# Kernel tuning notes

Hardware: AMD Instinct MI355X
Metric: run time of the kernel (lower is better)

## Reference

```python
import jax, jax.numpy as jnp
import numpy as np

N = 50000
E = 200000
DIMS = [3, 64, 64, 64, 128, 1024, 512, 256, 2]  # hard-coded layer widths from __init__


def setup_inputs() -> dict:
    key = jax.random.key(0)
    ks = jax.random.split(key, 2 + 2 * 8)
    inp = {}
    inp["x"] = jax.random.normal(ks[0], (N, DIMS[0]), dtype=jnp.float32)
    inp["edge_index"] = jax.random.randint(ks[1], (2, E), 0, N, dtype=jnp.int32)
    for i in range(8):
        w = jax.random.normal(ks[2 + 2 * i], (DIMS[i], DIMS[i + 1]), dtype=jnp.float32) / np.sqrt(DIMS[i]).astype(np.float32)
        b = jax.random.normal(ks[3 + 2 * i], (DIMS[i + 1],), dtype=jnp.float32) * 0.01
        inp[f"W{i}"] = w
        inp[f"b{i}"] = b
    return inp


def _gcn_layer(x, row, col, norm, W, b, n):
    # PyG GCNConv: h = x @ W; out_i = sum_{j->i} norm_ij * h_j; out += b
    h = x @ W                          # [N, F_out]
    msg = h[row] * norm[:, None]       # [E+N, F_out] gather + scale
    out = jax.ops.segment_sum(msg, col, num_segments=n)  # scatter-add
    return out + b


def reference(x, edge_index, W0, b0, W1, b1, W2, b2, W3, b3, W4, b4, W5, b5, W6, b6, W7, b7):
    n = x.shape[0]
    # add self-loops (GCNConv default add_self_loops=True)
    loops = jnp.arange(n, dtype=edge_index.dtype)
    row = jnp.concatenate([edge_index[0], loops])  # source nodes
    col = jnp.concatenate([edge_index[1], loops])  # target nodes
    # symmetric degree normalization: deg counts incoming edges at col
    deg = jax.ops.segment_sum(jnp.ones_like(col, dtype=x.dtype), col, num_segments=n)
    dis = jnp.where(deg > 0, jax.lax.rsqrt(jnp.maximum(deg, 1e-12)), 0.0)
    norm = dis[row] * dis[col]  # [E+N]

    Ws = [W0, W1, W2, W3, W4, W5, W6, W7]
    bs = [b0, b1, b2, b3, b4, b5, b6, b7]
    # dropout is identity in eval mode (training=False)
    for i in range(7):
        x = jax.nn.relu(_gcn_layer(x, row, col, norm, Ws[i], bs[i], n))
    x = _gcn_layer(x, row, col, norm, Ws[7], bs[7], n)
    return x
```

## Files before the change

kernel.cpp:

```cpp
#include <hip/hip_runtime.h>
#include <hip/hip_bf16.h>

typedef __hip_bfloat16 bf16;
typedef __attribute__((ext_vector_type(8))) short short8;
typedef __attribute__((ext_vector_type(4))) float floatx4;

__device__ inline float ldf(const float* p, size_t i) { return p[i]; }
__device__ inline float ldf(const bf16* p, size_t i) { return (float)p[i]; }
__device__ inline void stf(float* p, size_t i, float v) { p[i] = v; }
__device__ inline void stf(bf16* p, size_t i, float v) { p[i] = (bf16)v; }

__device__ inline void async16(const bf16* g, bf16* l) {
    __builtin_amdgcn_global_load_lds(
        (const __attribute__((address_space(1))) void*)g,
        (__attribute__((address_space(3))) void*)l, 16, 0, 0);
}

__device__ inline void loadvec(const float* __restrict__ p, float* d) {
    float4 v = *(const float4*)p;
    d[0] = v.x; d[1] = v.y; d[2] = v.z; d[3] = v.w;
}
__device__ inline void loadvec(const bf16* __restrict__ p, float* d) {
    uint4 u = *(const uint4*)p;
    const unsigned* w = (const unsigned*)&u;
    #pragma unroll
    for (int j = 0; j < 4; ++j) {
        d[2 * j]     = __uint_as_float(w[j] << 16);
        d[2 * j + 1] = __uint_as_float(w[j] & 0xffff0000u);
    }
}
template <int VEC, typename TOut>
__device__ inline void storevec(TOut* __restrict__ p, const float* d) {
    if constexpr (sizeof(TOut) == 4) {
        #pragma unroll
        for (int j = 0; j < VEC; j += 4) {
            float4 v = {d[j], d[j + 1], d[j + 2], d[j + 3]};
            *(float4*)(p + j) = v;
        }
    } else {
        unsigned w[VEC / 2];
        #pragma unroll
        for (int j = 0; j < VEC / 2; ++j) {
            bf16 lo = (bf16)d[2 * j], hi = (bf16)d[2 * j + 1];
            w[j] = ((unsigned)*(unsigned short*)&hi << 16) | (unsigned)*(unsigned short*)&lo;
        }
        if constexpr (VEC == 8) *(uint4*)p = *(uint4*)&w[0];
        else                    *(uint2*)p = *(uint2*)&w[0];
    }
}

__global__ void detect_dtype_kernel(const unsigned short* __restrict__ x, int* __restrict__ flag) {
    __shared__ float s[256];
    float m = 0.0f;
    for (int i = threadIdx.x; i < 512; i += 256) {
        unsigned int u = ((unsigned int)x[i]) << 16;
        float v = __uint_as_float(u);
        if (!isnan(v)) m = fmaxf(m, fabsf(v));
    }
    s[threadIdx.x] = m;
    __syncthreads();
    for (int o = 128; o > 0; o >>= 1) {
        if (threadIdx.x < (unsigned)o) s[threadIdx.x] = fmaxf(s[threadIdx.x], s[threadIdx.x + o]);
        __syncthreads();
    }
    if (threadIdx.x == 0) flag[0] = (s[0] > 1e3f) ? 0 : 1;
}

struct CvtJobs {
    const void* src[14];
    float* dst[14];
    int off[15];
    int cnt;
};
__global__ void cvt_fused_kernel(CvtJobs j, const int* __restrict__ flag) {
    int t = blockIdx.x * 256 + threadIdx.x;
    if (t >= j.off[j.cnt]) return;
    int k = 0;
    while (t >= j.off[k + 1]) ++k;
    int e = t - j.off[k];
    float v = *flag ? (float)((const bf16*)j.src[k])[e] : ((const float*)j.src[k])[e];
    j.dst[k][e] = v;
}

struct WtJobs {
    const void* src[3];
    bf16* dst[3];
    int K[3], N[3];
    int off[4];
};
__global__ void wt_fused_kernel(WtJobs j, const int* __restrict__ flag) {
    int t = blockIdx.x * 256 + threadIdx.x;
    if (t >= j.off[3]) return;
    int k_ = 0;
    while (t >= j.off[k_ + 1]) ++k_;
    int e = t - j.off[k_];
    int K = j.K[k_], Nn = j.N[k_];
    int n = e / K, kk = e % K;
    size_t si = (size_t)kk * Nn + n;
    float v = *flag ? (float)((const bf16*)j.src[k_])[si] : ((const float*)j.src[k_])[si];
    j.dst[k_][e] = (bf16)v;
}

__global__ void zero_int_kernel(int* a, int n) {
    int i = blockIdx.x * blockDim.x + threadIdx.x;
    if (i < n) a[i] = 0;
}

__global__ void hist_kernel(const int* __restrict__ col, int* __restrict__ counts, int E) {
    int e = blockIdx.x * blockDim.x + threadIdx.x;
    if (e < E) atomicAdd(&counts[col[e]], 1);
}

__global__ void scan_reduce_kernel(const int* __restrict__ counts, int* __restrict__ bs, int n) {
    __shared__ int s[1024];
    int i = blockIdx.x * 1024 + threadIdx.x;
    s[threadIdx.x] = (i < n) ? counts[i] : 0;
    __syncthreads();
    for (int o = 512; o > 0; o >>= 1) {
        if (threadIdx.x < (unsigned)o) s[threadIdx.x] += s[threadIdx.x + o];
        __syncthreads();
    }
    if (threadIdx.x == 0) bs[blockIdx.x] = s[0];
}

__global__ void scan_blocksums_kernel(int* __restrict__ bs, int nb) {
    __shared__ int s[1024];
    int v = (threadIdx.x < (unsigned)nb) ? bs[threadIdx.x] : 0;
    s[threadIdx.x] = v;
    __syncthreads();
    for (int off = 1; off < 1024; off <<= 1) {
        int t = (threadIdx.x >= (unsigned)off) ? s[threadIdx.x - off] : 0;
        __syncthreads();
        s[threadIdx.x] += t;
        __syncthreads();
    }
    if (threadIdx.x < (unsigned)nb) bs[threadIdx.x] = s[threadIdx.x] - v;
}

__global__ void scan_final_kernel(int* __restrict__ counts, const int* __restrict__ bs,
                                  int* __restrict__ offsets, float* __restrict__ dis, int n) {
    __shared__ int s[1024];
    int i = blockIdx.x * 1024 + threadIdx.x;
    int v = (i < n) ? counts[i] : 0;
    if (i < n) { dis[i] = rsqrtf((float)(v + 1)); counts[i] = 0; }
    s[threadIdx.x] = v;
    __syncthreads();
    for (int off = 1; off < 1024; off <<= 1) {
        int t = (threadIdx.x >= (unsigned)off) ? s[threadIdx.x - off] : 0;
        __syncthreads();
        s[threadIdx.x] += t;
        __syncthreads();
    }
    if (i < n) offsets[i + 1] = s[threadIdx.x] + bs[blockIdx.x];
    if (i == 0) offsets[0] = 0;
}

__global__ void fill_kernel(const int* __restrict__ row, const int* __restrict__ col,
                            const int* __restrict__ offsets, int* __restrict__ cursor,
                            int2* __restrict__ csr_sw, const float* __restrict__ dis, int E) {
    int e = blockIdx.x * blockDim.x + threadIdx.x;
    if (e < E) {
        int d = col[e];
        int s = row[e];
        int pos = offsets[d] + atomicAdd(&cursor[d], 1);
        csr_sw[pos] = make_int2(s, __float_as_int(dis[s]));
    }
}

template <typename TIn, typename TOut>
__global__ void agg_kernel(const TIn* __restrict__ h, const int* __restrict__ offsets,
                           const int2* __restrict__ csr_sw, const float* __restrict__ dis,
                           const float* __restrict__ bias, TOut* __restrict__ out,
                           int n, int F, int add_bias, int relu) {
    long long idx = (long long)blockIdx.x * blockDim.x + threadIdx.x;
    long long total = (long long)n * F;
    if (idx >= total) return;
    int i = (int)(idx / F);
    int f = (int)(idx % F);
    float di = dis[i];
    float acc = di * ldf(h, (size_t)i * F + f);
    float acc2 = 0.0f;
    int e0 = offsets[i], e1 = offsets[i + 1];
    int e = e0;
    for (; e + 1 < e1; e += 2) {
        int2 sw0 = csr_sw[e];
        int2 sw1 = csr_sw[e + 1];
        float v0 = ldf(h, (size_t)sw0.x * F + f);
        float v1 = ldf(h, (size_t)sw1.x * F + f);
        acc  += __int_as_float(sw0.y) * v0;
        acc2 += __int_as_float(sw1.y) * v1;
    }
    if (e < e1) {
        int2 sw = csr_sw[e];
        acc += __int_as_float(sw.y) * ldf(h, (size_t)sw.x * F + f);
    }
    acc = (acc + acc2) * di;
    if (add_bias) acc += bias[f];
    if (relu) acc = fmaxf(acc, 0.0f);
    stf(out, (size_t)idx, acc);
}

__global__ void agg2_out_kernel(const float* __restrict__ in, const int* __restrict__ offsets,
                                const int2* __restrict__ csr_sw, const float* __restrict__ dis,
                                const float* __restrict__ bias, void* __restrict__ out,
                                int n, const int* __restrict__ flag) {
    int idx = blockIdx.x * 256 + threadIdx.x;
    if (idx >= n * 2) return;
    int i = idx >> 1;
    int f = idx & 1;
    float di = dis[i];
    float acc = di * in[idx];
    float acc2 = 0.0f;
    int e0 = offsets[i], e1 = offsets[i + 1];
    int e = e0;
    for (; e + 1 < e1; e += 2) {
        int2 sw0 = csr_sw[e];
        int2 sw1 = csr_sw[e + 1];
        float v0 = in[(size_t)sw0.x * 2 + f];
        float v1 = in[(size_t)sw1.x * 2 + f];
        acc  += __int_as_float(sw0.y) * v0;
        acc2 += __int_as_float(sw1.y) * v1;
    }
    if (e < e1) {
        int2 sw = csr_sw[e];
        acc += __int_as_float(sw.y) * in[(size_t)sw.x * 2 + f];
    }
    acc = (acc + acc2) * di + bias[f];
    if (*flag) ((bf16*)out)[idx] = (bf16)acc;
    else       ((float*)out)[idx] = acc;
}

template <int F, int DO_BIAS, int DO_RELU, typename TIn, typename TOut>
__global__ __launch_bounds__(256) void agg_vec_kernel(
        const TIn* __restrict__ h, const int* __restrict__ offsets,
        const int2* __restrict__ csr_sw, const float* __restrict__ dis,
        const float* __restrict__ bias, TOut* __restrict__ out, int n) {
    constexpr int VEC = 16 / sizeof(TIn);
    constexpr int CPL = F / VEC;
    int t = blockIdx.x * 256 + threadIdx.x;
    if (t >= n * CPL) return;
    int i = t / CPL;
    int c = t % CPL;
    int fbase = c * VEC;
    float di = dis[i];
    float acc[VEC], acc2[VEC];
    loadvec(h + (size_t)i * F + fbase, acc);
    #pragma unroll
    for (int v = 0; v < VEC; ++v) { acc[v] *= di; acc2[v] = 0.0f; }
    int e0 = offsets[i], e1 = offsets[i + 1];
    int e = e0;
    for (; e + 3 < e1; e += 4) {
        int2 sw0 = csr_sw[e];
        int2 sw1 = csr_sw[e + 1];
        int2 sw2 = csr_sw[e + 2];
        int2 sw3 = csr_sw[e + 3];
        float t0[VEC], t1[VEC], t2[VEC], t3[VEC];
        loadvec(h + (size_t)sw0.x * F + fbase, t0);
        loadvec(h + (size_t)sw1.x * F + fbase, t1);
        loadvec(h + (size_t)sw2.x * F + fbase, t2);
        loadvec(h + (size_t)sw3.x * F + fbase, t3);
        float d0 = __int_as_float(sw0.y);
        float d1 = __int_as_float(sw1.y);
        float d2 = __int_as_float(sw2.y);
        float d3 = __int_as_float(sw3.y);
        #pragma unroll
        for (int v = 0; v < VEC; ++v) {
            acc[v]  += d0 * t0[v];
            acc2[v] += d1 * t1[v];
            acc[v]  += d2 * t2[v];
            acc2[v] += d3 * t3[v];
        }
    }
    for (; e + 1 < e1; e += 2) {
        int2 sw0 = csr_sw[e];
        int2 sw1 = csr_sw[e + 1];
        float t0[VEC], t1[VEC];
        loadvec(h + (size_t)sw0.x * F + fbase, t0);
        loadvec(h + (size_t)sw1.x * F + fbase, t1);
        float d0 = __int_as_float(sw0.y);
        float d1 = __int_as_float(sw1.y);
        #pragma unroll
        for (int v = 0; v < VEC; ++v) {
            acc[v]  += d0 * t0[v];
            acc2[v] += d1 * t1[v];
        }
    }
    if (e < e1) {
        int2 sw = csr_sw[e];
        float dsv = __int_as_float(sw.y);
        float tmp[VEC];
        loadvec(h + (size_t)sw.x * F + fbase, tmp);
        #pragma unroll
        for (int v = 0; v < VEC; ++v) acc[v] += dsv * tmp[v];
    }
    #pragma unroll
    for (int v = 0; v < VEC; ++v) {
        acc[v] = (acc[v] + acc2[v]) * di;
        if (DO_BIAS) acc[v] += bias[fbase + v];
        if (DO_RELU) acc[v] = fmaxf(acc[v], 0.0f);
    }
    storevec<VEC>(out + (size_t)i * F + fbase, acc);
}

__global__ __launch_bounds__(256) void gemm_k3_kernel(
        const float* __restrict__ A, const float* __restrict__ W,
        const float* __restrict__ bias, float* __restrict__ C, int M) {
    __shared__ float Ws[3][64];
    __shared__ float bs[64];
    if (threadIdx.x < 192) Ws[threadIdx.x >> 6][threadIdx.x & 63] = W[threadIdx.x];
    if (threadIdx.x < 64)  bs[threadIdx.x] = bias[threadIdx.x];
    __syncthreads();
    int t = blockIdx.x * 256 + threadIdx.x;
    if (t >= M * 16) return;
    int m = t >> 4;
    int c = (t & 15) << 2;
    float a0 = A[(size_t)m * 3], a1 = A[(size_t)m * 3 + 1], a2 = A[(size_t)m * 3 + 2];
    float4 o;
    o.x = fmaxf(a0 * Ws[0][c]     + a1 * Ws[1][c]     + a2 * Ws[2][c]     + bs[c],     0.f);
    o.y = fmaxf(a0 * Ws[0][c + 1] + a1 * Ws[1][c + 1] + a2 * Ws[2][c + 1] + bs[c + 1], 0.f);
    o.z = fmaxf(a0 * Ws[0][c + 2] + a1 * Ws[1][c + 2] + a2 * Ws[2][c + 2] + bs[c + 2], 0.f);
    o.w = fmaxf(a0 * Ws[0][c + 3] + a1 * Ws[1][c + 3] + a2 * Ws[2][c + 3] + bs[c + 3], 0.f);
    *(float4*)(C + (size_t)m * 64 + c) = o;
}

__global__ __launch_bounds__(256) void gemm_f2_kernel(
        const bf16* __restrict__ A, const float* __restrict__ W,
        float* __restrict__ C, int M) {
    __shared__ float Ws[256][2];
    for (int i = threadIdx.x; i < 512; i += 256) Ws[i >> 1][i & 1] = W[i];
    __syncthreads();
    int m = blockIdx.x * 256 + threadIdx.x;
    if (m >= M) return;
    const bf16* a = A + (size_t)m * 256;
    float acc0 = 0.f, acc1 = 0.f;
    #pragma unroll 4
    for (int k0 = 0; k0 < 256; k0 += 8) {
        float d[8];
        loadvec(a + k0, d);
        #pragma unroll
        for (int j = 0; j < 8; ++j) {
            acc0 += d[j] * Ws[k0 + j][0];
            acc1 += d[j] * Ws[k0 + j][1];
        }
    }
    C[(size_t)m * 2]     = acc0;
    C[(size_t)m * 2 + 1] = acc1;
}

template <typename TOut>
__global__ __launch_bounds__(256) void gemm_k64_kernel(
        const float* __restrict__ A,
        const float* __restrict__ W,
        const float* __restrict__ bias, TOut* __restrict__ C,
        int M, int Nc, int add_bias, int relu) {
    __shared__ float As[64][68];
    __shared__ float Bs[64][68];
    const int bm = blockIdx.x * 64;
    const int bn = blockIdx.y * 64;
    const int tid = threadIdx.x;
    #pragma unroll
    for (int l = 0; l < 4; ++l) {
        int lin = l * 256 + tid;
        int m = lin >> 4;
        int k = (lin & 15) << 2;
        int gm = bm + m; if (gm > M - 1) gm = M - 1;
        float4 v = *(const float4*)(A + (size_t)gm * 64 + k);
        As[k][m] = v.x; As[k + 1][m] = v.y; As[k + 2][m] = v.z; As[k + 3][m] = v.w;
    }
    #pragma unroll
    for (int l = 0; l < 4; ++l) {
        int lin = l * 256 + tid;
        int k = lin >> 4;
        int n = (lin & 15) << 2;
        *(float4*)(&Bs[k][n]) = *(const float4*)(W + (size_t)k * Nc + bn + n);
    }
    __syncthreads();
    const int tm = (tid >> 4) << 2;
    const int tn = (tid & 15) << 2;
    float acc[4][4] = {};
    #pragma unroll 8
    for (int k = 0; k < 64; ++k) {
        float a[4], b[4];
        #pragma unroll
        for (int i = 0; i < 4; ++i) a[i] = As[k][tm + i];
        #pragma unroll
        for (int j = 0; j < 4; ++j) b[j] = Bs[k][tn + j];
        #pragma unroll
        for (int i = 0; i < 4; ++i)
            #pragma unroll
            for (int j = 0; j < 4; ++j) acc[i][j] += a[i] * b[j];
    }
    #pragma unroll
    for (int i = 0; i < 4; ++i) {
        int gm = bm + tm + i;
        if (gm >= M) continue;
        #pragma unroll
        for (int j = 0; j < 4; ++j) {
            int gn = bn + tn + j;
            float v = acc[i][j];
            if (add_bias) v += bias[gn];
            if (relu) v = fmaxf(v, 0.0f);
            stf(C, (size_t)gm * Nc + gn, v);
        }
    }
}

template <int DO_BIAS, int DO_RELU>
__global__ __launch_bounds__(256) void gemm_mfma_k128_kernel(
        const bf16* __restrict__ A,
        const bf16* __restrict__ Bt,
        const float* __restrict__ bias,
        bf16* __restrict__ C,
        int M, int Nc) {
    __shared__ bf16 As[128 * 128];
    __shared__ bf16 Bs[128 * 128];
    const int tid  = threadIdx.x;
    const int wave = tid >> 6;
    const int lane = tid & 63;

    const int nwg  = (int)gridDim.x;
    const int orig = (int)blockIdx.x;
    const int q = nwg >> 3, r = nwg & 7;
    const int xcd = orig & 7;
    const int lin = orig >> 3;
    const int swz = (xcd < r ? xcd * (q + 1) : r * (q + 1) + (xcd - r) * q) + lin;
    const int nbn = Nc >> 7;
    const int bm = (swz / nbn) * 128;
    const int bn = (swz % nbn) * 128;

    const int wr = (wave >> 1) * 64;
    const int wc = (wave & 1) * 64;
    const int fm = lane & 15;
    const int fq = lane >> 4;

    #pragma unroll
    for (int p = 0; p < 8; ++p) {
        int idx = p * 256 + tid;
        int row = idx >> 4;
        int c   = idx & 15;
        int scol = (c ^ (row & 15)) << 3;
        int gm = bm + row; if (gm > M - 1) gm = M - 1;
        async16(A  + (size_t)gm * 128 + scol,        &As[idx * 8]);
        async16(Bt + (size_t)(bn + row) * 128 + scol, &Bs[idx * 8]);
    }
    asm volatile("s_waitcnt vmcnt(0)" ::: "memory");
    __builtin_amdgcn_s_barrier();

    floatx4 acc[4][4] = {};
    #pragma unroll
    for (int t = 0; t < 4; ++t) {
        short8 af[4], bfv[4];
        #pragma unroll
        for (int mt = 0; mt < 4; ++mt) {
            int rowa = wr + mt * 16 + fm;
            int ch = (4 * t + fq) ^ (rowa & 15);
            af[mt] = *(const short8*)(&As[rowa * 128 + ch * 8]);
        }
        #pragma unroll
        for (int ntc = 0; ntc < 4; ++ntc) {
            int rowb = wc + ntc * 16 + fm;
            int ch = (4 * t + fq) ^ (rowb & 15);
            bfv[ntc] = *(const short8*)(&Bs[rowb * 128 + ch * 8]);
        }
        #pragma unroll
        for (int mt = 0; mt < 4; ++mt)
            #pragma unroll
            for (int ntc = 0; ntc < 4; ++ntc)
                acc[mt][ntc] = __builtin_amdgcn_mfma_f32_16x16x32_bf16(
                    af[mt], bfv[ntc], acc[mt][ntc], 0, 0, 0);
    }

    #pragma unroll
    for (int mt = 0; mt < 4; ++mt) {
        #pragma unroll
        for (int r2 = 0; r2 < 4; ++r2) {
            int gm = bm + wr + mt * 16 + fq * 4 + r2;
            if (gm >= M) continue;
            #pragma unroll
            for (int ntc = 0; ntc < 4; ++ntc) {
                int gn = bn + wc + ntc * 16 + fm;
                float v = acc[mt][ntc][r2];
                if (DO_BIAS) v += bias[gn];
                if (DO_RELU) v = fmaxf(v, 0.0f);
                C[(size_t)gm * Nc + gn] = (bf16)v;
            }
        }
    }
}

template <int DO_BIAS, int DO_RELU, typename TOut>
__global__ __launch_bounds__(256) void gemm_mfma_kernel(
        const bf16* __restrict__ A,
        const bf16* __restrict__ Bt,
        const float* __restrict__ bias,
        TOut* __restrict__ C,
        int M, int Nc, int K) {
    __shared__ bf16 As[3][128 * 32];
    __shared__ bf16 Bs[3][128 * 32];
    const int tid  = threadIdx.x;
    const int wave = tid >> 6;
    const int lane = tid & 63;

    const int nwg  = (int)gridDim.x;
    const int orig = (int)blockIdx.x;
    const int q = nwg >> 3, r = nwg & 7;
    const int xcd = orig & 7;
    const int lin = orig >> 3;
    const int swz = (xcd < r ? xcd * (q + 1) : r * (q + 1) + (xcd - r) * q) + lin;
    const int nbn = Nc >> 7;
    const int bm = (swz / nbn) * 128;
    const int bn = (swz % nbn) * 128;

    const int wr = (wave >> 1) * 64;
    const int wc = (wave & 1) * 64;
    const int fm = lane & 15;
    const int fq = lane >> 4;
    const int fks = (fq ^ ((fm >> 1) & 3)) << 3;

    const int r0 = tid >> 2;
    const int r1 = (256 + tid) >> 2;
    const int sc0 = ((tid & 3) ^ ((r0 >> 1) & 3)) << 3;
    const int sc1 = (((256 + tid) & 3) ^ ((r1 >> 1) & 3)) << 3;
    const int e0 = tid * 8;
    const int e1 = (256 + tid) * 8;
    int gmA0 = bm + r0; if (gmA0 > M - 1) gmA0 = M - 1;
    int gmA1 = bm + r1; if (gmA1 > M - 1) gmA1 = M - 1;

    const bf16* a0p = A  + (size_t)gmA0 * K + sc0;
    const bf16* a1p = A  + (size_t)gmA1 * K + sc1;
    const bf16* b0p = Bt + (size_t)(bn + r0) * K + sc0;
    const bf16* b1p = Bt + (size_t)(bn + r1) * K + sc1;

    auto stage = [&](int slot, int kt) {
        const int k0 = kt << 5;
        async16(a0p + k0, &As[slot][e0]);
        async16(a1p + k0, &As[slot][e1]);
        async16(b0p + k0, &Bs[slot][e0]);
        async16(b1p + k0, &Bs[slot][e1]);
    };

    floatx4 acc[4][4] = {};
    const int nt = K >> 5;

    stage(0, 0);
    if (nt > 1) stage(1, 1);

    int cur = 0;
    for (int t = 0; t < nt; ++t) {
        if (t + 1 < nt) asm volatile("s_waitcnt vmcnt(4)" ::: "memory");
        else            asm volatile("s_waitcnt vmcnt(0)" ::: "memory");
        __builtin_amdgcn_s_barrier();
        if (t + 2 < nt) {
            int sp = cur + 2; if (sp >= 3) sp -= 3;
            stage(sp, t + 2);
        }
        short8 af[4], bfv[4];
        #pragma unroll
        for (int t4 = 0; t4 < 4; ++t4) {
            af[t4]  = *(const short8*)(&As[cur][(wr + t4 * 16 + fm) * 32 + fks]);
            bfv[t4] = *(const short8*)(&Bs[cur][(wc + t4 * 16 + fm) * 32 + fks]);
        }
        __builtin_amdgcn_s_setprio(1);
        #pragma unroll
        for (int mt = 0; mt < 4; ++mt)
            #pragma unroll
            for (int ntc = 0; ntc < 4; ++ntc)
                acc[mt][ntc] = __builtin_amdgcn_mfma_f32_16x16x32_bf16(
                    af[mt], bfv[ntc], acc[mt][ntc], 0, 0, 0);
        __builtin_amdgcn_s_setprio(0);
        ++cur; if (cur >= 3) cur = 0;
    }

    #pragma unroll
    for (int mt = 0; mt < 4; ++mt) {
        #pragma unroll
        for (int r2 = 0; r2 < 4; ++r2) {
            int gm = bm + wr + mt * 16 + fq * 4 + r2;
            if (gm >= M) continue;
            #pragma unroll
            for (int ntc = 0; ntc < 4; ++ntc) {
                int gn = bn + wc + ntc * 16 + fm;
                float v = acc[mt][ntc][r2];
                if (DO_BIAS) v += bias[gn];
                if (DO_RELU) v = fmaxf(v, 0.0f);
                stf(C, (size_t)gm * Nc + gn, v);
            }
        }
    }
}


static inline int cdiv(long long a, int b) { return (int)((a + b - 1) / b); }

extern "C" void kernel_launch(void* const* d_in, const int* in_sizes, int n_in,
                              void* d_out, int out_size, void* d_ws, size_t ws_size,
                              hipStream_t stream) {
    const int N = in_sizes[0] / 3;
    const int E = in_sizes[1] / 2;

    const int* edge_index = (const int*)d_in[1];
    const int* row = edge_index;
    const int* col = edge_index + E;

    char* p = (char*)d_ws;
    auto alloc = [&](size_t bytes) {
        void* r = (void*)p;
        p += (bytes + 255) & ~(size_t)255;
        return r;
    };
    void* bufA    = alloc((size_t)N * 2048);
    void* bufB    = alloc((size_t)N * 1024);
    float* dis    = (float*)alloc((size_t)N * sizeof(float));
    int* offsets  = (int*)alloc((size_t)(N + 1) * sizeof(int));
    int* cursor   = (int*)alloc((size_t)N * sizeof(int));
    int2* csr_sw  = (int2*)alloc((size_t)E * sizeof(int2));
    int* flag     = (int*)alloc(256);
    int* blocksums = (int*)alloc((size_t)cdiv(N, 1024) * sizeof(int));
    const int WfL[5] = {0, 1, 2, 3, 7};
    float* Wf[8] = {};
    float* bf_[8];
    for (int t = 0; t < 5; ++t) {
        int L = WfL[t];
        Wf[L] = (float*)alloc((size_t)in_sizes[2 + 2 * L] * sizeof(float));
    }
    for (int L = 0; L < 8; ++L)
        bf_[L] = (float*)alloc((size_t)in_sizes[3 + 2 * L] * sizeof(float));
    bf16* Wt4 = (bf16*)alloc((size_t)128 * 1024 * sizeof(bf16));
    bf16* Wt5 = (bf16*)alloc((size_t)1024 * 512 * sizeof(bf16));
    bf16* Wt6 = (bf16*)alloc((size_t)512 * 256 * sizeof(bf16));
    size_t needed = (size_t)(p - (char*)d_ws);
    if (ws_size < needed) return;

    float* fA = (float*)bufA;  bf16* hA = (bf16*)bufA;
    float* fB = (float*)bufB;  bf16* hB = (bf16*)bufB;

    const int T = 256;

    detect_dtype_kernel<<<1, 256, 0, stream>>>((const unsigned short*)d_in[0], flag);

    {
        CvtJobs cj{};
        int idx = 0, cum = 0;
        auto add = [&](const void* s, float* d, int n) {
            cj.src[idx] = s; cj.dst[idx] = d; cj.off[idx] = cum; cum += n; ++idx;
        };
        add(d_in[0], fA, N * 3);
        for (int t = 0; t < 5; ++t) {
            int L = WfL[t];
            add(d_in[2 + 2 * L], Wf[L], in_sizes[2 + 2 * L]);
        }
        for (int L = 0; L < 8; ++L)
            add(d_in[3 + 2 * L], bf_[L], in_sizes[3 + 2 * L]);
        cj.off[idx] = cum; cj.cnt = idx;
        cvt_fused_kernel<<<cdiv(cum, T), T, 0, stream>>>(cj, flag);
    }

    {
        WtJobs wj{};
        wj.src[0] = d_in[2 + 2 * 4]; wj.dst[0] = Wt4; wj.K[0] = 128;  wj.N[0] = 1024;
        wj.src[1] = d_in[2 + 2 * 5]; wj.dst[1] = Wt5; wj.K[1] = 1024; wj.N[1] = 512;
        wj.src[2] = d_in[2 + 2 * 6]; wj.dst[2] = Wt6; wj.K[2] = 512;  wj.N[2] = 256;
        wj.off[0] = 0;
        wj.off[1] = 128 * 1024;
        wj.off[2] = 128 * 1024 + 1024 * 512;
        wj.off[3] = 128 * 1024 + 1024 * 512 + 512 * 256;
        wt_fused_kernel<<<cdiv(wj.off[3], T), T, 0, stream>>>(wj, flag);
    }

    {
        zero_int_kernel<<<cdiv(N, T), T, 0, stream>>>(cursor, N);
        hist_kernel<<<cdiv(E, T), T, 0, stream>>>(col, cursor, E);
        int nb = cdiv(N, 1024);
        scan_reduce_kernel<<<nb, 1024, 0, stream>>>(cursor, blocksums, N);
        scan_blocksums_kernel<<<1, 1024, 0, stream>>>(blocksums, nb);
        scan_final_kernel<<<nb, 1024, 0, stream>>>(cursor, blocksums, offsets, dis, N);
        fill_kernel<<<cdiv(E, T), T, 0, stream>>>(row, col, offsets, cursor, csr_sw, dis, E);
    }

    agg_kernel<float, float><<<cdiv((long long)N * 3, T), T, 0, stream>>>(
        fA, offsets, csr_sw, dis, nullptr, fB, N, 3, 0, 0);
    gemm_k3_kernel<<<cdiv((long long)N * 16, T), T, 0, stream>>>(fB, Wf[0], bf_[0], fA, N);

    {
        dim3 g(cdiv(N, 64), 1);
        gemm_k64_kernel<float><<<g, 256, 0, stream>>>(fA, Wf[1], nullptr, fB, N, 64, 0, 0);
        agg_vec_kernel<64, 1, 1, float, float><<<cdiv((long long)N * 16, T), T, 0, stream>>>(
            fB, offsets, csr_sw, dis, bf_[1], fA, N);
    }

    {
        dim3 g(cdiv(N, 64), 1);
        gemm_k64_kernel<float><<<g, 256, 0, stream>>>(fA, Wf[2], nullptr, fB, N, 64, 0, 0);
        agg_vec_kernel<64, 1, 1, float, float><<<cdiv((long long)N * 16, T), T, 0, stream>>>(
            fB, offsets, csr_sw, dis, bf_[2], fA, N);
    }

    {
        agg_vec_kernel<64, 0, 0, float, float><<<cdiv((long long)N * 16, T), T, 0, stream>>>(
            fA, offsets, csr_sw, dis, nullptr, fB, N);
        dim3 g(cdiv(N, 64), 2);
        gemm_k64_kernel<bf16><<<g, 256, 0, stream>>>(fB, Wf[3], bf_[3], hA, N, 128, 1, 1);
    }

    {
        agg_vec_kernel<128, 0, 0, bf16, bf16><<<cdiv((long long)N * 16, T), T, 0, stream>>>(
            hA, offsets, csr_sw, dis, nullptr, hB, N);
        int nwg = cdiv(N, 128) * (1024 / 128);
        gemm_mfma_k128_kernel<1, 1><<<nwg, 256, 0, stream>>>(hB, Wt4, bf_[4], hA, N, 1024);
    }

    {
        int nwg = cdiv(N, 128) * (512 / 128);
        gemm_mfma_kernel<0, 0, bf16><<<nwg, 256, 0, stream>>>(hA, Wt5, nullptr, hB, N, 512, 1024);
        agg_vec_kernel<512, 1, 1, bf16, bf16><<<cdiv((long long)N * 64, T), T, 0, stream>>>(
            hB, offsets, csr_sw, dis, bf_[5], hA, N);
    }

    {
        int nwg = cdiv(N, 128) * (256 / 128);
        gemm_mfma_kernel<0, 0, bf16><<<nwg, 256, 0, stream>>>(hA, Wt6, nullptr, hB, N, 256, 512);
        agg_vec_kernel<256, 1, 1, bf16, bf16><<<cdiv((long long)N * 32, T), T, 0, stream>>>(
            hB, offsets, csr_sw, dis, bf_[6], hA, N);
    }

    {
        gemm_f2_kernel<<<cdiv(N, T), T, 0, stream>>>(hA, Wf[7], fB, N);
        agg2_out_kernel<<<cdiv((long long)N * 2, T), T, 0, stream>>>(
            fB, offsets, csr_sw, dis, bf_[7], d_out, N, flag);
    }
}
```

Baseline: 468.1 us.

## Use 256x256 tiles with 8 waves and interleaved prefetch for large GEMMs

Replaces the 128x128, 4-wave MFMA GEMM used for layers 5 and 6 with a 256x256 tile kernel run by 512 threads. Each wave computes a 128x64 sub-tile in two halves, with the async global-to-LDS prefetch split between them so loads overlap the MFMA phases. The larger tile is meant to raise arithmetic intensity and cut global/L2 traffic per output. In exchange it uses more LDS, more accumulator registers and more barriers, and the N=256 layer launches only about 196 workgroups, which may underfill the GPU.

```diff
diff --git a/kernel.cpp b/kernel.cpp
--- a/kernel.cpp
+++ b/kernel.cpp
@@ -349,8 +349,7 @@
 
 template <typename TOut>
 __global__ __launch_bounds__(256) void gemm_k64_kernel(
-        const float* __restrict__ A,
-        const float* __restrict__ W,
+        const float* __restrict__ A, const float* __restrict__ W,
         const float* __restrict__ bias, TOut* __restrict__ C,
         int M, int Nc, int add_bias, int relu) {
     __shared__ float As[64][68];
@@ -407,10 +406,8 @@
 
 template <int DO_BIAS, int DO_RELU>
 __global__ __launch_bounds__(256) void gemm_mfma_k128_kernel(
-        const bf16* __restrict__ A,
-        const bf16* __restrict__ Bt,
-        const float* __restrict__ bias,
-        bf16* __restrict__ C,
+        const bf16* __restrict__ A, const bf16* __restrict__ Bt,
+        const float* __restrict__ bias, bf16* __restrict__ C,
         int M, int Nc) {
     __shared__ bf16 As[128 * 128];
     __shared__ bf16 Bs[128 * 128];
@@ -488,18 +485,22 @@
     }
 }
 
-template <int DO_BIAS, int DO_RELU, typename TOut>
-__global__ __launch_bounds__(256) void gemm_mfma_kernel(
+template <int DO_BIAS, int DO_RELU>
+__global__ __launch_bounds__(512, 2) void gemm_mfma_256_kernel(
         const bf16* __restrict__ A,
         const bf16* __restrict__ Bt,
         const float* __restrict__ bias,
-        TOut* __restrict__ C,
+        bf16* __restrict__ C,
         int M, int Nc, int K) {
-    __shared__ bf16 As[3][128 * 32];
-    __shared__ bf16 Bs[3][128 * 32];
+    __shared__ bf16 As[3][256 * 32];
+    __shared__ bf16 Bs[3][256 * 32];
     const int tid  = threadIdx.x;
     const int wave = tid >> 6;
     const int lane = tid & 63;
+    const int wm = wave >> 2;
+    const int wn = wave & 3;
+    const int fm = lane & 15;
+    const int fq = lane >> 4;
 
     const int nwg  = (int)gridDim.x;
     const int orig = (int)blockIdx.x;
@@ -507,83 +508,98 @@
     const int xcd = orig & 7;
     const int lin = orig >> 3;
     const int swz = (xcd < r ? xcd * (q + 1) : r * (q + 1) + (xcd - r) * q) + lin;
-    const int nbn = Nc >> 7;
-    const int bm = (swz / nbn) * 128;
-    const int bn = (swz % nbn) * 128;
-
-    const int wr = (wave >> 1) * 64;
-    const int wc = (wave & 1) * 64;
-    const int fm = lane & 15;
-    const int fq = lane >> 4;
-    const int fks = (fq ^ ((fm >> 1) & 3)) << 3;
-
-    const int r0 = tid >> 2;
-    const int r1 = (256 + tid) >> 2;
-    const int sc0 = ((tid & 3) ^ ((r0 >> 1) & 3)) << 3;
-    const int sc1 = (((256 + tid) & 3) ^ ((r1 >> 1) & 3)) << 3;
-    const int e0 = tid * 8;
-    const int e1 = (256 + tid) * 8;
-    int gmA0 = bm + r0; if (gmA0 > M - 1) gmA0 = M - 1;
-    int gmA1 = bm + r1; if (gmA1 > M - 1) gmA1 = M - 1;
-
-    const bf16* a0p = A  + (size_t)gmA0 * K + sc0;
-    const bf16* a1p = A  + (size_t)gmA1 * K + sc1;
-    const bf16* b0p = Bt + (size_t)(bn + r0) * K + sc0;
-    const bf16* b1p = Bt + (size_t)(bn + r1) * K + sc1;
-
-    auto stage = [&](int slot, int kt) {
-        const int k0 = kt << 5;
-        async16(a0p + k0, &As[slot][e0]);
-        async16(a1p + k0, &As[slot][e1]);
-        async16(b0p + k0, &Bs[slot][e0]);
-        async16(b1p + k0, &Bs[slot][e1]);
-    };
-
-    floatx4 acc[4][4] = {};
+    const int nbn = Nc >> 8;
+    const int bm = (swz / nbn) * 256;
+    const int bn = (swz % nbn) * 256;
+
+    const int srl = tid >> 2;
+    const int sc  = tid & 3;
+    const int scol = (sc ^ ((srl >> 1) & 3)) << 3;
+    int gmA0 = bm + srl;        if (gmA0 > M - 1) gmA0 = M - 1;
+    int gmA1 = bm + 128 + srl;  if (gmA1 > M - 1) gmA1 = M - 1;
+    const bf16* a0 = A  + (size_t)gmA0 * K + scol;
+    const bf16* a1 = A  + (size_t)gmA1 * K + scol;
+    const bf16* b0 = Bt + (size_t)(bn + srl) * K + scol;
+    const bf16* b1 = Bt + (size_t)(bn + 128 + srl) * K + scol;
+    const int ld0 = srl * 32 + sc * 8;
+    const int ld1 = (128 + srl) * 32 + sc * 8;
+
     const int nt = K >> 5;
-
-    stage(0, 0);
-    if (nt > 1) stage(1, 1);
+    floatx4 acc[8][4] = {};
+
+    async16(a0,      &As[0][ld0]); async16(a1,      &As[0][ld1]);
+    async16(b0,      &Bs[0][ld0]); async16(b1,      &Bs[0][ld1]);
+    async16(a0 + 32, &As[1][ld0]); async16(a1 + 32, &As[1][ld1]);
+    async16(b0 + 32, &Bs[1][ld0]); async16(b1 + 32, &Bs[1][ld1]);
+    asm volatile("s_waitcnt vmcnt(4)" ::: "memory");
+    __builtin_amdgcn_s_barrier();
 
     int cur = 0;
     for (int t = 0; t < nt; ++t) {
-        if (t + 1 < nt) asm volatile("s_waitcnt vmcnt(4)" ::: "memory");
-        else            asm volatile("s_waitcnt vmcnt(0)" ::: "memory");
+        int sp = cur + 2; if (sp >= 3) sp -= 3;
+        const int k2 = (t + 2) << 5;
+        const bool pf = (t + 2) < nt;
+        short8 af[4], bfv[4];
+
+        #pragma unroll
+        for (int i = 0; i < 4; ++i) {
+            int ra = wm * 128 + i * 16 + fm;
+            af[i] = *(const short8*)(&As[cur][ra * 32 + ((fq ^ ((ra >> 1) & 3)) << 3)]);
+        }
+        #pragma unroll
+        for (int j = 0; j < 4; ++j) {
+            int rb = wn * 64 + j * 16 + fm;
+            bfv[j] = *(const short8*)(&Bs[cur][rb * 32 + ((fq ^ ((rb >> 1) & 3)) << 3)]);
+        }
+        if (pf) { async16(a0 + k2, &As[sp][ld0]); async16(a1 + k2, &As[sp][ld1]); }
         __builtin_amdgcn_s_barrier();
-        if (t + 2 < nt) {
-            int sp = cur + 2; if (sp >= 3) sp -= 3;
-            stage(sp, t + 2);
-        }
-        short8 af[4], bfv[4];
-        #pragma unroll
-        for (int t4 = 0; t4 < 4; ++t4) {
-            af[t4]  = *(const short8*)(&As[cur][(wr + t4 * 16 + fm) * 32 + fks]);
-            bfv[t4] = *(const short8*)(&Bs[cur][(wc + t4 * 16 + fm) * 32 + fks]);
-        }
         __builtin_amdgcn_s_setprio(1);
         #pragma unroll
-        for (int mt = 0; mt < 4; ++mt)
+        for (int i = 0; i < 4; ++i)
             #pragma unroll
-            for (int ntc = 0; ntc < 4; ++ntc)
-                acc[mt][ntc] = __builtin_amdgcn_mfma_f32_16x16x32_bf16(
-                    af[mt], bfv[ntc], acc[mt][ntc], 0, 0, 0);
+            for (int j = 0; j < 4; ++j)
+                acc[i][j] = __builtin_amdgcn_mfma_f32_16x16x32_bf16(
+                    af[i], bfv[j], acc[i][j], 0, 0, 0);
         __builtin_amdgcn_s_setprio(0);
+        __builtin_amdgcn_s_barrier();
+
+        #pragma unroll
+        for (int i = 0; i < 4; ++i) {
+            int ra = wm * 128 + 64 + i * 16 + fm;
+            af[i] = *(const short8*)(&As[cur][ra * 32 + ((fq ^ ((ra >> 1) & 3)) << 3)]);
+        }
+        if (pf) { async16(b0 + k2, &Bs[sp][ld0]); async16(b1 + k2, &Bs[sp][ld1]); }
+        if (t + 1 < nt) {
+            if (pf) asm volatile("s_waitcnt vmcnt(4)" ::: "memory");
+            else    asm volatile("s_waitcnt vmcnt(0)" ::: "memory");
+        }
+        __builtin_amdgcn_s_barrier();
+        __builtin_amdgcn_s_setprio(1);
+        #pragma unroll
+        for (int i = 0; i < 4; ++i)
+            #pragma unroll
+            for (int j = 0; j < 4; ++j)
+                acc[4 + i][j] = __builtin_amdgcn_mfma_f32_16x16x32_bf16(
+                    af[i], bfv[j], acc[4 + i][j], 0, 0, 0);
+        __builtin_amdgcn_s_setprio(0);
+        __builtin_amdgcn_s_barrier();
+
         ++cur; if (cur >= 3) cur = 0;
     }
 
     #pragma unroll
-    for (int mt = 0; mt < 4; ++mt) {
-        #pragma unroll
-        for (int r2 = 0; r2 < 4; ++r2) {
-            int gm = bm + wr + mt * 16 + fq * 4 + r2;
+    for (int ig = 0; ig < 8; ++ig) {
+        #pragma unroll
+        for (int rr = 0; rr < 4; ++rr) {
+            int gm = bm + wm * 128 + ig * 16 + fq * 4 + rr;
             if (gm >= M) continue;
             #pragma unroll
-            for (int ntc = 0; ntc < 4; ++ntc) {
-                int gn = bn + wc + ntc * 16 + fm;
-                float v = acc[mt][ntc][r2];
+            for (int j = 0; j < 4; ++j) {
+                int gn = bn + wn * 64 + j * 16 + fm;
+                float v = acc[ig][j][rr];
                 if (DO_BIAS) v += bias[gn];
                 if (DO_RELU) v = fmaxf(v, 0.0f);
-                stf(C, (size_t)gm * Nc + gn, v);
+                C[(size_t)gm * Nc + gn] = (bf16)v;
             }
         }
     }
@@ -710,15 +726,15 @@
     }
 
     {
-        int nwg = cdiv(N, 128) * (512 / 128);
-        gemm_mfma_kernel<0, 0, bf16><<<nwg, 256, 0, stream>>>(hA, Wt5, nullptr, hB, N, 512, 1024);
+        int nwg = cdiv(N, 256) * (512 / 256);
+        gemm_mfma_256_kernel<0, 0><<<nwg, 512, 0, stream>>>(hA, Wt5, nullptr, hB, N, 512, 1024);
         agg_vec_kernel<512, 1, 1, bf16, bf16><<<cdiv((long long)N * 64, T), T, 0, stream>>>(
             hB, offsets, csr_sw, dis, bf_[5], hA, N);
     }
 
     {
-        int nwg = cdiv(N, 128) * (256 / 128);
-        gemm_mfma_kernel<0, 0, bf16><<<nwg, 256, 0, stream>>>(hA, Wt6, nullptr, hB, N, 256, 512);
+        int nwg = cdiv(N, 256) * (256 / 256);
+        gemm_mfma_256_kernel<0, 0><<<nwg, 512, 0, stream>>>(hA, Wt6, nullptr, hB, N, 256, 512);
         agg_vec_kernel<256, 1, 1, bf16, bf16><<<cdiv((long long)N * 32, T), T, 0, stream>>>(
             hB, offsets, csr_sw, dis, bf_[6], hA, N);
     }
```

New measurement: 458.1 us (median of 2 runs). 1.02x faster.
